# Kernel optimization log

Hardware: AMD Instinct MI355X
Metric: run time of the kernel (lower is better)

The kernel has to match this reference:

```python
import jax, jax.numpy as jnp
import numpy as np

N_NODES = 100000
N_EDGES = 600000
IN_DIM = 128
EDGE_DIM = 32
HIDDEN = 128
NUM_CLASSES = 2


def _glorot(key, shape):
    fan_in, fan_out = shape[0], shape[1]
    lim = float(np.sqrt(6.0 / (fan_in + fan_out)))
    return jax.random.uniform(key, shape, jnp.float32, -lim, lim)


def setup_inputs() -> dict:
    key = jax.random.key(0)
    ks = jax.random.split(key, 16)
    inp = {
        "x": jax.random.normal(ks[0], (N_NODES, IN_DIM), jnp.float32),
        "edge_index": jax.random.randint(ks[1], (2, N_EDGES), 0, N_NODES, jnp.int64),
        "edge_attr": jax.random.normal(ks[2], (N_EDGES, EDGE_DIM), jnp.float32),
        # SAGEConv layer 1 (edge-aware): edge proj, neighbor lin, self lin
        "We1": _glorot(ks[3], (EDGE_DIM, IN_DIM)),
        "be1": jnp.zeros((IN_DIM,), jnp.float32),
        "Wl1": _glorot(ks[4], (IN_DIM, HIDDEN)),
        "bl1": jnp.zeros((HIDDEN,), jnp.float32),
        "Wr1": _glorot(ks[5], (IN_DIM, HIDDEN)),
        "br1": jnp.zeros((HIDDEN,), jnp.float32),
        # SAGEConv layer 2
        "We2": _glorot(ks[6], (EDGE_DIM, HIDDEN)),
        "be2": jnp.zeros((HIDDEN,), jnp.float32),
        "Wl2": _glorot(ks[7], (HIDDEN, HIDDEN)),
        "bl2": jnp.zeros((HIDDEN,), jnp.float32),
        "Wr2": _glorot(ks[8], (HIDDEN, HIDDEN)),
        "br2": jnp.zeros((HIDDEN,), jnp.float32),
        # Edge MLP predictor: Linear(2*hidden, hidden) -> ReLU -> Linear(hidden, num_classes)
        "Wp1": _glorot(ks[9], (2 * HIDDEN, HIDDEN)),
        "bp1": jnp.zeros((HIDDEN,), jnp.float32),
        "Wp2": _glorot(ks[10], (HIDDEN, NUM_CLASSES)),
        "bp2": jnp.zeros((NUM_CLASSES,), jnp.float32),
    }
    return inp


def _sage_conv(x, src, dst, edge_attr, We, be, Wl, bl, Wr, br):
    # Edge-aware message: m_ij = x_j + proj(e_ij); mean-aggregate over dst;
    # out_i = mean_agg @ Wl + x_i @ Wr  (GraphSAGE mean aggregator with edge fusion)
    msg = x[src] + edge_attr @ We + be                       # [E, d]
    agg = jax.ops.segment_sum(msg, dst, num_segments=N_NODES)  # [N, d]
    deg = jax.ops.segment_sum(jnp.ones((msg.shape[0],), msg.dtype), dst, num_segments=N_NODES)
    mean = agg / jnp.maximum(deg, 1.0)[:, None]
    return mean @ Wl + bl + x @ Wr + br


def reference(x, edge_index, edge_attr,
              We1, be1, Wl1, bl1, Wr1, br1,
              We2, be2, Wl2, bl2, Wr2, br2,
              Wp1, bp1, Wp2, bp2):
    src, dst = edge_index[0], edge_index[1]
    h = jax.nn.relu(_sage_conv(x, src, dst, edge_attr, We1, be1, Wl1, bl1, Wr1, br1))
    h = jax.nn.relu(_sage_conv(h, src, dst, edge_attr, We2, be2, Wl2, bl2, Wr2, br2))
    # Edge predictor: gather endpoints, concat, MLP -> logits [E, num_classes]
    he = jnp.concatenate([h[src], h[dst]], axis=-1)
    return jax.nn.relu(he @ Wp1 + bp1) @ Wp2 + bp2
```

## Files before the change

kernel.cpp:

```cpp
#include <hip/hip_runtime.h>

#define N_NODES 100000
#define N_EDGES 600000
#define IN_DIM 128
#define EDGE_DIM 32
#define HIDDEN 128
#define NUM_CLASSES 2
#define NBLK 391

typedef __attribute__((ext_vector_type(4))) float f32x4;
typedef _Float16 f16x2 __attribute__((ext_vector_type(2)));
typedef _Float16 f16x4 __attribute__((ext_vector_type(4)));
typedef _Float16 f16x8 __attribute__((ext_vector_type(8)));

__global__ void hist_kernel(const int* __restrict__ dst, int* __restrict__ cnt) {
    int e = blockIdx.x * blockDim.x + threadIdx.x;
    if (e < N_EDGES) atomicAdd(&cnt[dst[e]], 1);
}

__global__ void scan1_kernel(const int* __restrict__ cnt,
                             int* __restrict__ scanout, int* __restrict__ bsum) {
    __shared__ int s[256];
    int tid = threadIdx.x;
    int i = blockIdx.x * 256 + tid;
    int v = (i < N_NODES) ? cnt[i] : 0;
    s[tid] = v;
    __syncthreads();
#pragma unroll
    for (int off = 1; off < 256; off <<= 1) {
        int t = 0;
        if (tid >= off) t = s[tid - off];
        __syncthreads();
        if (tid >= off) s[tid] += t;
        __syncthreads();
    }
    if (i < N_NODES) scanout[i] = s[tid];
    if (tid == 255) bsum[blockIdx.x] = s[255];
}

__global__ void scan2_kernel(int* __restrict__ bsum) {
    __shared__ int s[512];
    int tid = threadIdx.x;
    int v = (tid < NBLK) ? bsum[tid] : 0;
    s[tid] = v;
    __syncthreads();
#pragma unroll
    for (int off = 1; off < 512; off <<= 1) {
        int t = 0;
        if (tid >= off) t = s[tid - off];
        __syncthreads();
        if (tid >= off) s[tid] += t;
        __syncthreads();
    }
    if (tid < NBLK) bsum[tid] = s[tid] - v;
}

__global__ void scan3_kernel(const int* __restrict__ cnt,
                             const int* __restrict__ scanout,
                             const int* __restrict__ bsum,
                             int* __restrict__ rowptr, int* __restrict__ cur) {
    int i = blockIdx.x * 256 + threadIdx.x;
    if (i < N_NODES) {
        int excl = scanout[i] + bsum[i >> 8] - cnt[i];
        rowptr[i] = excl;
        cur[i] = excl;
    }
    if (i == 0) rowptr[N_NODES] = N_EDGES;
}

__global__ void fill_kernel(const int* __restrict__ src, const int* __restrict__ dst,
                            int* __restrict__ cur, int2* __restrict__ pk,
                            int* __restrict__ pdst) {
    int e = blockIdx.x * blockDim.x + threadIdx.x;
    if (e < N_EDGES) {
        int d = dst[e];
        int pos = atomicAdd(&cur[d], 1);
        int2 v;
        v.x = src[e];
        v.y = e;
        pk[pos] = v;
        pdst[pos] = d;
    }
}

__global__ void xb_kernel(const float* __restrict__ x, _Float16* __restrict__ xb) {
    int i = blockIdx.x * 256 + threadIdx.x;
    if (i < N_NODES * HIDDEN / 2) {
        float2 v = ((const float2*)x)[i];
        f16x2 o;
        o.x = (_Float16)v.x;
        o.y = (_Float16)v.y;
        *(f16x2*)&xb[i * 2] = o;
    }
}

__global__ void wewl_kernel(const float* __restrict__ We, const float* __restrict__ be,
                            const float* __restrict__ Wl,
                            float* __restrict__ WeWl, float* __restrict__ beWl) {
    int idx = blockIdx.x * 256 + threadIdx.x;
    if (idx >= 33 * 128) return;
    int r = idx >> 7;
    int n = idx & 127;
    float s = 0.f;
    if (r < 32) {
        for (int j = 0; j < 128; ++j) s += We[r * 128 + j] * Wl[j * 128 + n];
        WeWl[r * 128 + n] = s;
    } else {
        for (int j = 0; j < 128; ++j) s += be[j] * Wl[j * 128 + n];
        beWl[n] = s;
    }
}

__global__ void wbig_swizzle_kernel(const float* __restrict__ Wl,
                                    const float* __restrict__ Wr,
                                    const float* __restrict__ WeWl,
                                    _Float16* __restrict__ Wbs) {
    int idx = blockIdx.x * 256 + threadIdx.x;
    if (idx >= 8 * 9 * 64 * 8) return;
    int j = idx & 7;
    int lane = (idx >> 3) & 63;
    int rem = idx >> 9;
    int ks = rem % 9;
    int nt = rem / 9;
    int k = ks * 32 + ((lane >> 4) & 3) * 8 + j;
    int n = nt * 16 + (lane & 15);
    float v = (k < 128) ? Wl[k * 128 + n]
            : (k < 256) ? Wr[(k - 128) * 128 + n]
                        : WeWl[(k - 256) * 128 + n];
    Wbs[idx] = (_Float16)v;
}

template <bool EA>
__global__ __launch_bounds__(256) void agg_kernel_t(const _Float16* __restrict__ xin,
                                                    const int* __restrict__ rowptr,
                                                    const int2* __restrict__ pk,
                                                    const float* __restrict__ ea,
                                                    _Float16* __restrict__ meanb,
                                                    _Float16* __restrict__ eamb) {
    int wid = blockIdx.x * 4 + (threadIdx.x >> 6);
    int lane = threadIdx.x & 63;
    int node = lane >> 3;
    int slot = lane & 7;
    int half = lane >> 5;
    int k = lane & 31;
    int n0 = wid * 8;

    int rp = rowptr[n0 + (lane < 9 ? lane : 8)];
    int s_n = __shfl(rp, node);
    int e_n = __shfl(rp, node + 1);
    int c_n = e_n - s_n; c_n = c_n > 8 ? 8 : c_n;
    int pos = s_n + (slot < c_n ? slot : 0);
    pos = pos < N_EDGES ? pos : N_EDGES - 1;
    int2 pv = pk[pos];

    float accx[8], accy[8], eacc[8];
#pragma unroll
    for (int i = 0; i < 8; ++i) {
        accx[i] = 0.f; accy[i] = 0.f;
        if (EA) eacc[i] = 0.f;
    }

#pragma unroll
    for (int i = 0; i < 8; ++i) {
        int di = __shfl(rp, i + 1) - __shfl(rp, i);
        int ci = di > 8 ? 8 : di;
        f16x2 r[8];
#pragma unroll
        for (int u = 0; u < 8; ++u) {
            int s = __shfl(pv.x, i * 8 + u);
            r[u] = *(const f16x2*)&xin[s * HIDDEN + lane * 2];
        }
        float g[4];
        if (EA) {
#pragma unroll
            for (int up = 0; up < 4; ++up) {
                int eid = __shfl(pv.y, i * 8 + 2 * up + half);
                g[up] = ea[eid * EDGE_DIM + k];
            }
        }
#pragma unroll
        for (int u = 0; u < 8; ++u)
            if (u < ci) { accx[i] += (float)r[u].x; accy[i] += (float)r[u].y; }
        if (EA) {
#pragma unroll
            for (int up = 0; up < 4; ++up)
                if (2 * up + half < ci) eacc[i] += g[up];
        }
    }

#pragma unroll
    for (int i = 0; i < 8; ++i) {
        int si = __shfl(rp, i);
        int ei = __shfl(rp, i + 1);
        int p = si + 8;
        if (p < ei) {
            do {
                int c = ei - p; c = c > 8 ? 8 : c;
                int2 pv2 = pk[p + (slot < c ? slot : 0)];
                f16x2 r[8];
#pragma unroll
                for (int u = 0; u < 8; ++u) {
                    int s = __shfl(pv2.x, u);
                    r[u] = *(const f16x2*)&xin[s * HIDDEN + lane * 2];
                }
                float g[4];
                if (EA) {
#pragma unroll
                    for (int up = 0; up < 4; ++up) {
                        int eid = __shfl(pv2.y, 2 * up + half);
                        g[up] = ea[eid * EDGE_DIM + k];
                    }
                }
#pragma unroll
                for (int u = 0; u < 8; ++u)
                    if (u < c) { accx[i] += (float)r[u].x; accy[i] += (float)r[u].y; }
                if (EA) {
#pragma unroll
                    for (int up = 0; up < 4; ++up)
                        if (2 * up + half < c) eacc[i] += g[up];
                }
                p += c;
            } while (p < ei);
        }
    }

    float dinv[8];
#pragma unroll
    for (int i = 0; i < 8; ++i) {
        int di = __shfl(rp, i + 1) - __shfl(rp, i);
        dinv[i] = 1.f / (float)(di > 1 ? di : 1);
    }
#pragma unroll
    for (int i = 0; i < 8; ++i) {
        f16x2 o;
        o.x = (_Float16)(accx[i] * dinv[i]);
        o.y = (_Float16)(accy[i] * dinv[i]);
        *(f16x2*)&meanb[(n0 + i) * HIDDEN + lane * 2] = o;
    }
    if (EA) {
#pragma unroll
        for (int i = 0; i < 8; ++i) eacc[i] += __shfl_xor(eacc[i], 32);
#pragma unroll
        for (int j = 0; j < 4; ++j) {
            float v  = half ? eacc[4 + j] : eacc[j];
            float dv = half ? dinv[4 + j] : dinv[j];
            int i = half * 4 + j;
            eamb[(n0 + i) * EDGE_DIM + k] = (_Float16)(v * dv);
        }
    }
}

#define APITCH 296
__global__ __launch_bounds__(256) void node_gemm_kernel(
        const _Float16* __restrict__ meanb,
        const _Float16* __restrict__ xb,
        const _Float16* __restrict__ eamb,
        const _Float16* __restrict__ Wbs,
        const int* __restrict__ rowptr,
        const float* __restrict__ bl, const float* __restrict__ br,
        const float* __restrict__ beWl,
        _Float16* __restrict__ outb) {
    __shared__ _Float16 s_a[64 * APITCH];
    __shared__ float s_bias[128];
    __shared__ float s_bw[128];
    __shared__ int s_deg[64];
    int t = threadIdx.x;
    int n0 = blockIdx.x * 64;

    if (t < 128) {
        s_bias[t] = bl[t] + br[t];
        s_bw[t] = beWl[t];
    } else if (t < 192) {
        int m = t - 128;
        int n = n0 + m;
        n = n < N_NODES ? n : N_NODES - 1;
        s_deg[m] = rowptr[n + 1] - rowptr[n];
    }
    for (int i = t; i < 64 * 16; i += 256) {
        int row = i >> 4, seg = i & 15;
        int n = n0 + row;
        n = n < N_NODES ? n : N_NODES - 1;
        *(f16x8*)&s_a[row * APITCH + seg * 8] = *(const f16x8*)&meanb[n * HIDDEN + seg * 8];
        *(f16x8*)&s_a[row * APITCH + 128 + seg * 8] = *(const f16x8*)&xb[n * HIDDEN + seg * 8];
    }
    for (int i = t; i < 64 * 4; i += 256) {
        int row = i >> 2, seg = i & 3;
        int n = n0 + row;
        n = n < N_NODES ? n : N_NODES - 1;
        *(f16x8*)&s_a[row * APITCH + 256 + seg * 8] = *(const f16x8*)&eamb[n * EDGE_DIM + seg * 8];
    }
    __syncthreads();

    int wave = t >> 6;
    int lane = t & 63;
    int col = lane & 15;
    int kgrp = lane >> 4;

    f32x4 acc[8];
#pragma unroll
    for (int nt = 0; nt < 8; ++nt) acc[nt] = (f32x4){0.f, 0.f, 0.f, 0.f};

    const f16x8* __restrict__ Wb = (const f16x8*)Wbs;
#pragma unroll
    for (int ks = 0; ks < 9; ++ks) {
        f16x8 afrag = *(const f16x8*)&s_a[(wave * 16 + col) * APITCH + ks * 32 + kgrp * 8];
#pragma unroll
        for (int nt = 0; nt < 8; ++nt) {
            f16x8 bfrag = Wb[(nt * 9 + ks) * 64 + lane];
            acc[nt] = __builtin_amdgcn_mfma_f32_16x16x32_f16(afrag, bfrag, acc[nt], 0, 0, 0);
        }
    }

#pragma unroll
    for (int nt = 0; nt < 8; ++nt) {
        int feat = nt * 16 + col;
        float b = s_bias[feat];
        float bw = s_bw[feat];
#pragma unroll
        for (int r = 0; r < 4; ++r) {
            int m = wave * 16 + kgrp * 4 + r;
            int n = n0 + m;
            float v = acc[nt][r] + b + (s_deg[m] > 0 ? bw : 0.f);
            v = v > 0.f ? v : 0.f;
            if (n < N_NODES) outb[n * HIDDEN + feat] = (_Float16)v;
        }
    }
}

__global__ void wp1uv_swizzle_kernel(const float* __restrict__ Wp1,
                                     _Float16* __restrict__ Wuv) {
    int idx = blockIdx.x * 256 + threadIdx.x;
    if (idx >= 32768) return;
    int j = idx & 7;
    int lane = (idx >> 3) & 63;
    int ks = (idx >> 9) & 3;
    int nt = (idx >> 11) & 15;
    int k = ks * 32 + ((lane >> 4) & 3) * 8 + j;
    int n = nt * 16 + (lane & 15);
    float v = (n < 128) ? Wp1[k * 128 + n] : Wp1[(128 + k) * 128 + (n - 128)];
    Wuv[idx] = (_Float16)v;
}

#define UPITCH 136
__global__ __launch_bounds__(256) void uv_gemm_kernel(
        const _Float16* __restrict__ h,
        const _Float16* __restrict__ Wuv,
        const float* __restrict__ bp1,
        _Float16* __restrict__ UV) {
    __shared__ _Float16 s_a[64 * UPITCH];
    __shared__ float s_bias[256];
    int t = threadIdx.x;
    int n0 = blockIdx.x * 64;

    s_bias[t] = (t < 128) ? bp1[t] : 0.f;
    for (int i = t; i < 64 * 16; i += 256) {
        int row = i >> 4, seg = i & 15;
        int n = n0 + row;
        n = n < N_NODES ? n : N_NODES - 1;
        *(f16x8*)&s_a[row * UPITCH + seg * 8] = *(const f16x8*)&h[n * HIDDEN + seg * 8];
    }
    __syncthreads();

    int wave = t >> 6;
    int lane = t & 63;
    int col = lane & 15;
    int kgrp = lane >> 4;

    f32x4 acc[16];
#pragma unroll
    for (int nt = 0; nt < 16; ++nt) acc[nt] = (f32x4){0.f, 0.f, 0.f, 0.f};

    const f16x8* __restrict__ Wb = (const f16x8*)Wuv;
#pragma unroll
    for (int ks = 0; ks < 4; ++ks) {
        f16x8 afrag = *(const f16x8*)&s_a[(wave * 16 + col) * UPITCH + ks * 32 + kgrp * 8];
#pragma unroll
        for (int nt = 0; nt < 16; ++nt) {
            f16x8 bfrag = Wb[(nt * 4 + ks) * 64 + lane];
            acc[nt] = __builtin_amdgcn_mfma_f32_16x16x32_f16(afrag, bfrag, acc[nt], 0, 0, 0);
        }
    }

#pragma unroll
    for (int nt = 0; nt < 16; ++nt) {
        int feat = nt * 16 + col;
        float b = s_bias[feat];
#pragma unroll
        for (int r = 0; r < 4; ++r) {
            int m = wave * 16 + kgrp * 4 + r;
            int n = n0 + m;
            if (n < N_NODES) UV[n * 256 + feat] = (_Float16)(acc[nt][r] + b);
        }
    }
}

__global__ __launch_bounds__(256) void edge_pred_kernel(
        const _Float16* __restrict__ UV,
        const int2* __restrict__ pk,
        const int* __restrict__ pdst,
        const float* __restrict__ Wp2,
        const float* __restrict__ bp2,
        float* __restrict__ out) {
    int t = threadIdx.x;
    int wave = t >> 6;
    int lane = t & 63;
    int slot = lane >> 5;
    int k4 = (lane & 31) * 4;

    float4 wa = *(const float4*)&Wp2[k4 * 2];
    float4 wb = *(const float4*)&Wp2[k4 * 2 + 4];
    float b0 = bp2[0], b1 = bp2[1];

    int e0 = blockIdx.x * 32 + wave * 8;

    int2 pv[4];
    int dn[4];
#pragma unroll
    for (int u = 0; u < 4; ++u) {
        int pos = e0 + 2 * u + slot;
        pv[u] = pk[pos];
        dn[u] = pdst[pos];
    }
    f16x4 uu[4], vv[4];
#pragma unroll
    for (int u = 0; u < 4; ++u) {
        uu[u] = *(const f16x4*)&UV[pv[u].x * 256 + k4];
        vv[u] = *(const f16x4*)&UV[dn[u] * 256 + 128 + k4];
    }

    float p0[4], p1[4];
#pragma unroll
    for (int u = 0; u < 4; ++u) {
        float z0 = (float)uu[u].x + (float)vv[u].x; z0 = z0 > 0.f ? z0 : 0.f;
        float z1 = (float)uu[u].y + (float)vv[u].y; z1 = z1 > 0.f ? z1 : 0.f;
        float z2 = (float)uu[u].z + (float)vv[u].z; z2 = z2 > 0.f ? z2 : 0.f;
        float z3 = (float)uu[u].w + (float)vv[u].w; z3 = z3 > 0.f ? z3 : 0.f;
        p0[u] = z0 * wa.x + z1 * wa.z + z2 * wb.x + z3 * wb.z;
        p1[u] = z0 * wa.y + z1 * wa.w + z2 * wb.y + z3 * wb.w;
    }
#pragma unroll
    for (int m = 1; m < 32; m <<= 1) {
#pragma unroll
        for (int u = 0; u < 4; ++u) {
            p0[u] += __shfl_xor(p0[u], m);
            p1[u] += __shfl_xor(p1[u], m);
        }
    }
    if ((lane & 31) == 0) {
#pragma unroll
        for (int u = 0; u < 4; ++u) {
            float2 o;
            o.x = p0[u] + b0;
            o.y = p1[u] + b1;
            *(float2*)&out[pv[u].y * 2] = o;
        }
    }
}

extern "C" void kernel_launch(void* const* d_in, const int* in_sizes, int n_in,
                              void* d_out, int out_size, void* d_ws, size_t ws_size,
                              hipStream_t stream) {
    const float* x   = (const float*)d_in[0];
    const int*   ei  = (const int*)d_in[1];
    const float* ea  = (const float*)d_in[2];
    const float* We1 = (const float*)d_in[3];
    const float* be1 = (const float*)d_in[4];
    const float* Wl1 = (const float*)d_in[5];
    const float* bl1 = (const float*)d_in[6];
    const float* Wr1 = (const float*)d_in[7];
    const float* br1 = (const float*)d_in[8];
    const float* We2 = (const float*)d_in[9];
    const float* be2 = (const float*)d_in[10];
    const float* Wl2 = (const float*)d_in[11];
    const float* bl2 = (const float*)d_in[12];
    const float* Wr2 = (const float*)d_in[13];
    const float* br2 = (const float*)d_in[14];
    const float* Wp1 = (const float*)d_in[15];
    const float* bp1 = (const float*)d_in[16];
    const float* Wp2 = (const float*)d_in[17];
    const float* bp2 = (const float*)d_in[18];
    float* out = (float*)d_out;

    const int* src = ei;
    const int* dst = ei + N_EDGES;

    char* ws = (char*)d_ws;
    int*   cnt     = (int*)(ws + 0);
    int*   scanout = (int*)(ws + 409600);
    int*   bsum    = (int*)(ws + 819200);
    int*   rowptr  = (int*)(ws + 827392);
    int*   cur     = (int*)(ws + 1236992);
    int2*  pk      = (int2*)(ws + 1646592);
    float* WeWl1   = (float*)(ws + 6447104);
    float* beWl1   = (float*)(ws + 6463488);
    float* WeWl2   = (float*)(ws + 6464000);
    float* beWl2   = (float*)(ws + 6480384);
    _Float16* eamb = (_Float16*)(ws + 6480896);
    _Float16* xb   = (_Float16*)(ws + 12880896);
    _Float16* meanb= (_Float16*)(ws + 38480896);
    _Float16* UV   = (_Float16*)(ws + 12880896);
    _Float16* h1b  = (_Float16*)(ws + 64080896);
    _Float16* h2b  = (_Float16*)(ws + 89680896);
    _Float16* Wbs1 = (_Float16*)(ws + 115280896);
    _Float16* Wbs2 = (_Float16*)(ws + 115354624);
    _Float16* Wuv  = (_Float16*)(ws + 115428352);
    int*   pdst    = (int*)(ws + 115493888);

    const int EB = (N_EDGES + 255) / 256;

    hipMemsetAsync(cnt, 0, N_NODES * sizeof(int), stream);
    hist_kernel<<<EB, 256, 0, stream>>>(dst, cnt);
    scan1_kernel<<<NBLK, 256, 0, stream>>>(cnt, scanout, bsum);
    scan2_kernel<<<1, 512, 0, stream>>>(bsum);
    scan3_kernel<<<NBLK, 256, 0, stream>>>(cnt, scanout, bsum, rowptr, cur);
    fill_kernel<<<EB, 256, 0, stream>>>(src, dst, cur, pk, pdst);

    wewl_kernel<<<17, 256, 0, stream>>>(We1, be1, Wl1, WeWl1, beWl1);
    wewl_kernel<<<17, 256, 0, stream>>>(We2, be2, Wl2, WeWl2, beWl2);
    xb_kernel<<<(N_NODES * HIDDEN / 2 + 255) / 256, 256, 0, stream>>>(x, xb);
    wbig_swizzle_kernel<<<144, 256, 0, stream>>>(Wl1, Wr1, WeWl1, Wbs1);
    wbig_swizzle_kernel<<<144, 256, 0, stream>>>(Wl2, Wr2, WeWl2, Wbs2);
    wp1uv_swizzle_kernel<<<128, 256, 0, stream>>>(Wp1, Wuv);

    agg_kernel_t<true><<<N_NODES / 32, 256, 0, stream>>>(xb, rowptr, pk, ea, meanb, eamb);
    node_gemm_kernel<<<(N_NODES + 63) / 64, 256, 0, stream>>>(
        meanb, xb, eamb, Wbs1, rowptr, bl1, br1, beWl1, h1b);

    agg_kernel_t<false><<<N_NODES / 32, 256, 0, stream>>>(h1b, rowptr, pk, nullptr, meanb, nullptr);
    node_gemm_kernel<<<(N_NODES + 63) / 64, 256, 0, stream>>>(
        meanb, h1b, eamb, Wbs2, rowptr, bl2, br2, beWl2, h2b);

    uv_gemm_kernel<<<(N_NODES + 63) / 64, 256, 0, stream>>>(h2b, Wuv, bp1, UV);
    edge_pred_kernel<<<N_EDGES / 32, 256, 0, stream>>>(UV, pk, pdst, Wp2, bp2, out);
}
```

Measured before the change: 495.7 us.

## Fuse neighbor aggregation into node GEMM and use MFMA for edge predictor

Merges the separate mean-aggregation and node GEMM kernels into one per-layer kernel that writes the aggregated means straight into shared memory. This removes the meanb global round trip and two launches. The edge predictor's second linear layer is now a padded 16x16x32 MFMA over a pre-swizzled fp16 Wp2 instead of per-lane dot products with shuffle reductions. The trade-offs are fewer waves doing the gather per node-GEMM block, which lowers parallelism in the latency-bound gather, and extra fp16 rounding of the ReLU activations in the predictor.

```diff
diff --git a/kernel.cpp b/kernel.cpp
--- a/kernel.cpp
+++ b/kernel.cpp
@@ -130,133 +130,15 @@
     Wbs[idx] = (_Float16)v;
 }
 
+#define APITCH 296
 template <bool EA>
-__global__ __launch_bounds__(256) void agg_kernel_t(const _Float16* __restrict__ xin,
-                                                    const int* __restrict__ rowptr,
-                                                    const int2* __restrict__ pk,
-                                                    const float* __restrict__ ea,
-                                                    _Float16* __restrict__ meanb,
-                                                    _Float16* __restrict__ eamb) {
-    int wid = blockIdx.x * 4 + (threadIdx.x >> 6);
-    int lane = threadIdx.x & 63;
-    int node = lane >> 3;
-    int slot = lane & 7;
-    int half = lane >> 5;
-    int k = lane & 31;
-    int n0 = wid * 8;
-
-    int rp = rowptr[n0 + (lane < 9 ? lane : 8)];
-    int s_n = __shfl(rp, node);
-    int e_n = __shfl(rp, node + 1);
-    int c_n = e_n - s_n; c_n = c_n > 8 ? 8 : c_n;
-    int pos = s_n + (slot < c_n ? slot : 0);
-    pos = pos < N_EDGES ? pos : N_EDGES - 1;
-    int2 pv = pk[pos];
-
-    float accx[8], accy[8], eacc[8];
-#pragma unroll
-    for (int i = 0; i < 8; ++i) {
-        accx[i] = 0.f; accy[i] = 0.f;
-        if (EA) eacc[i] = 0.f;
-    }
-
-#pragma unroll
-    for (int i = 0; i < 8; ++i) {
-        int di = __shfl(rp, i + 1) - __shfl(rp, i);
-        int ci = di > 8 ? 8 : di;
-        f16x2 r[8];
-#pragma unroll
-        for (int u = 0; u < 8; ++u) {
-            int s = __shfl(pv.x, i * 8 + u);
-            r[u] = *(const f16x2*)&xin[s * HIDDEN + lane * 2];
-        }
-        float g[4];
-        if (EA) {
-#pragma unroll
-            for (int up = 0; up < 4; ++up) {
-                int eid = __shfl(pv.y, i * 8 + 2 * up + half);
-                g[up] = ea[eid * EDGE_DIM + k];
-            }
-        }
-#pragma unroll
-        for (int u = 0; u < 8; ++u)
-            if (u < ci) { accx[i] += (float)r[u].x; accy[i] += (float)r[u].y; }
-        if (EA) {
-#pragma unroll
-            for (int up = 0; up < 4; ++up)
-                if (2 * up + half < ci) eacc[i] += g[up];
-        }
-    }
-
-#pragma unroll
-    for (int i = 0; i < 8; ++i) {
-        int si = __shfl(rp, i);
-        int ei = __shfl(rp, i + 1);
-        int p = si + 8;
-        if (p < ei) {
-            do {
-                int c = ei - p; c = c > 8 ? 8 : c;
-                int2 pv2 = pk[p + (slot < c ? slot : 0)];
-                f16x2 r[8];
-#pragma unroll
-                for (int u = 0; u < 8; ++u) {
-                    int s = __shfl(pv2.x, u);
-                    r[u] = *(const f16x2*)&xin[s * HIDDEN + lane * 2];
-                }
-                float g[4];
-                if (EA) {
-#pragma unroll
-                    for (int up = 0; up < 4; ++up) {
-                        int eid = __shfl(pv2.y, 2 * up + half);
-                        g[up] = ea[eid * EDGE_DIM + k];
-                    }
-                }
-#pragma unroll
-                for (int u = 0; u < 8; ++u)
-                    if (u < c) { accx[i] += (float)r[u].x; accy[i] += (float)r[u].y; }
-                if (EA) {
-#pragma unroll
-                    for (int up = 0; up < 4; ++up)
-                        if (2 * up + half < c) eacc[i] += g[up];
-                }
-                p += c;
-            } while (p < ei);
-        }
-    }
-
-    float dinv[8];
-#pragma unroll
-    for (int i = 0; i < 8; ++i) {
-        int di = __shfl(rp, i + 1) - __shfl(rp, i);
-        dinv[i] = 1.f / (float)(di > 1 ? di : 1);
-    }
-#pragma unroll
-    for (int i = 0; i < 8; ++i) {
-        f16x2 o;
-        o.x = (_Float16)(accx[i] * dinv[i]);
-        o.y = (_Float16)(accy[i] * dinv[i]);
-        *(f16x2*)&meanb[(n0 + i) * HIDDEN + lane * 2] = o;
-    }
-    if (EA) {
-#pragma unroll
-        for (int i = 0; i < 8; ++i) eacc[i] += __shfl_xor(eacc[i], 32);
-#pragma unroll
-        for (int j = 0; j < 4; ++j) {
-            float v  = half ? eacc[4 + j] : eacc[j];
-            float dv = half ? dinv[4 + j] : dinv[j];
-            int i = half * 4 + j;
-            eamb[(n0 + i) * EDGE_DIM + k] = (_Float16)(v * dv);
-        }
-    }
-}
-
-#define APITCH 296
-__global__ __launch_bounds__(256) void node_gemm_kernel(
-        const _Float16* __restrict__ meanb,
-        const _Float16* __restrict__ xb,
-        const _Float16* __restrict__ eamb,
+__global__ __launch_bounds__(256) void fused_layer_kernel(
+        const _Float16* __restrict__ xin,
+        const int* __restrict__ rowptr,
+        const int2* __restrict__ pk,
+        const float* __restrict__ ea,
+        _Float16* __restrict__ eamb,
         const _Float16* __restrict__ Wbs,
-        const int* __restrict__ rowptr,
         const float* __restrict__ bl, const float* __restrict__ br,
         const float* __restrict__ beWl,
         _Float16* __restrict__ outb) {
@@ -266,33 +148,150 @@
     __shared__ int s_deg[64];
     int t = threadIdx.x;
     int n0 = blockIdx.x * 64;
-
-    if (t < 128) {
-        s_bias[t] = bl[t] + br[t];
-        s_bw[t] = beWl[t];
-    } else if (t < 192) {
-        int m = t - 128;
-        int n = n0 + m;
-        n = n < N_NODES ? n : N_NODES - 1;
-        s_deg[m] = rowptr[n + 1] - rowptr[n];
-    }
+    int wave = t >> 6;
+    int lane = t & 63;
+
+    if (t < 128) { s_bias[t] = bl[t] + br[t]; s_bw[t] = beWl[t]; }
+
     for (int i = t; i < 64 * 16; i += 256) {
         int row = i >> 4, seg = i & 15;
-        int n = n0 + row;
-        n = n < N_NODES ? n : N_NODES - 1;
-        *(f16x8*)&s_a[row * APITCH + seg * 8] = *(const f16x8*)&meanb[n * HIDDEN + seg * 8];
-        *(f16x8*)&s_a[row * APITCH + 128 + seg * 8] = *(const f16x8*)&xb[n * HIDDEN + seg * 8];
-    }
-    for (int i = t; i < 64 * 4; i += 256) {
-        int row = i >> 2, seg = i & 3;
-        int n = n0 + row;
-        n = n < N_NODES ? n : N_NODES - 1;
-        *(f16x8*)&s_a[row * APITCH + 256 + seg * 8] = *(const f16x8*)&eamb[n * EDGE_DIM + seg * 8];
+        int n = n0 + row; n = n < N_NODES ? n : N_NODES - 1;
+        *(f16x8*)&s_a[row * APITCH + 128 + seg * 8] = *(const f16x8*)&xin[n * HIDDEN + seg * 8];
+    }
+    if (!EA) {
+        for (int i = t; i < 64 * 4; i += 256) {
+            int row = i >> 2, seg = i & 3;
+            int n = n0 + row; n = n < N_NODES ? n : N_NODES - 1;
+            *(f16x8*)&s_a[row * APITCH + 256 + seg * 8] = *(const f16x8*)&eamb[n * EDGE_DIM + seg * 8];
+        }
+    }
+
+    int node = lane >> 3;
+    int slot = lane & 7;
+    int half = lane >> 5;
+    int kk = lane & 31;
+
+#pragma unroll 1
+    for (int g = 0; g < 2; ++g) {
+        int ng = n0 + wave * 16 + g * 8;
+        int rpi = ng + (lane < 9 ? lane : 8);
+        rpi = rpi < N_NODES ? rpi : N_NODES;
+        int rp = rowptr[rpi];
+        int s_n = __shfl(rp, node);
+        int e_n = __shfl(rp, node + 1);
+        int c_n = e_n - s_n; c_n = c_n > 8 ? 8 : c_n;
+        int pos = s_n + (slot < c_n ? slot : 0);
+        pos = pos < N_EDGES ? pos : N_EDGES - 1;
+        int2 pv = pk[pos];
+
+        float accx[8], accy[8], eacc[8];
+#pragma unroll
+        for (int i = 0; i < 8; ++i) {
+            accx[i] = 0.f; accy[i] = 0.f;
+            if (EA) eacc[i] = 0.f;
+        }
+
+#pragma unroll
+        for (int i = 0; i < 8; ++i) {
+            int di = __shfl(rp, i + 1) - __shfl(rp, i);
+            int ci = di > 8 ? 8 : di;
+            f16x2 r[8];
+#pragma unroll
+            for (int u = 0; u < 8; ++u) {
+                int s = __shfl(pv.x, i * 8 + u);
+                r[u] = *(const f16x2*)&xin[s * HIDDEN + lane * 2];
+            }
+            float gg[4];
+            if (EA) {
+#pragma unroll
+                for (int up = 0; up < 4; ++up) {
+                    int eid = __shfl(pv.y, i * 8 + 2 * up + half);
+                    gg[up] = ea[eid * EDGE_DIM + kk];
+                }
+            }
+#pragma unroll
+            for (int u = 0; u < 8; ++u)
+                if (u < ci) { accx[i] += (float)r[u].x; accy[i] += (float)r[u].y; }
+            if (EA) {
+#pragma unroll
+                for (int up = 0; up < 4; ++up)
+                    if (2 * up + half < ci) eacc[i] += gg[up];
+            }
+        }
+
+#pragma unroll
+        for (int i = 0; i < 8; ++i) {
+            int si = __shfl(rp, i);
+            int ei2 = __shfl(rp, i + 1);
+            int p = si + 8;
+            if (p < ei2) {
+                do {
+                    int c = ei2 - p; c = c > 8 ? 8 : c;
+                    int2 pv2 = pk[p + (slot < c ? slot : 0)];
+                    f16x2 r[8];
+#pragma unroll
+                    for (int u = 0; u < 8; ++u) {
+                        int s = __shfl(pv2.x, u);
+                        r[u] = *(const f16x2*)&xin[s * HIDDEN + lane * 2];
+                    }
+                    float gg[4];
+                    if (EA) {
+#pragma unroll
+                        for (int up = 0; up < 4; ++up) {
+                            int eid = __shfl(pv2.y, 2 * up + half);
+                            gg[up] = ea[eid * EDGE_DIM + kk];
+                        }
+                    }
+#pragma unroll
+                    for (int u = 0; u < 8; ++u)
+                        if (u < c) { accx[i] += (float)r[u].x; accy[i] += (float)r[u].y; }
+                    if (EA) {
+#pragma unroll
+                        for (int up = 0; up < 4; ++up)
+                            if (2 * up + half < c) eacc[i] += gg[up];
+                    }
+                    p += c;
+                } while (p < ei2);
+            }
+        }
+
+        float dinv[8];
+#pragma unroll
+        for (int i = 0; i < 8; ++i) {
+            int di = __shfl(rp, i + 1) - __shfl(rp, i);
+            dinv[i] = 1.f / (float)(di > 1 ? di : 1);
+        }
+#pragma unroll
+        for (int i = 0; i < 8; ++i) {
+            int row = wave * 16 + g * 8 + i;
+            f16x2 o;
+            o.x = (_Float16)(accx[i] * dinv[i]);
+            o.y = (_Float16)(accy[i] * dinv[i]);
+            *(f16x2*)&s_a[row * APITCH + lane * 2] = o;
+        }
+        {
+            int li = lane < 8 ? lane : 0;
+            int dd = __shfl(rp, li + 1) - __shfl(rp, li);
+            if (lane < 8) s_deg[wave * 16 + g * 8 + lane] = dd;
+        }
+        if (EA) {
+#pragma unroll
+            for (int i = 0; i < 8; ++i) eacc[i] += __shfl_xor(eacc[i], 32);
+#pragma unroll
+            for (int j = 0; j < 4; ++j) {
+                float v  = half ? eacc[4 + j] : eacc[j];
+                float dv = half ? dinv[4 + j] : dinv[j];
+                int i = half * 4 + j;
+                int row = wave * 16 + g * 8 + i;
+                _Float16 hv = (_Float16)(v * dv);
+                s_a[row * APITCH + 256 + kk] = hv;
+                int nn = ng + i;
+                if (nn < N_NODES) eamb[nn * EDGE_DIM + kk] = hv;
+            }
+        }
     }
     __syncthreads();
 
-    int wave = t >> 6;
-    int lane = t & 63;
     int col = lane & 15;
     int kgrp = lane >> 4;
 
@@ -328,17 +327,28 @@
 }
 
 __global__ void wp1uv_swizzle_kernel(const float* __restrict__ Wp1,
-                                     _Float16* __restrict__ Wuv) {
+                                     const float* __restrict__ Wp2,
+                                     _Float16* __restrict__ Wuv,
+                                     _Float16* __restrict__ Wp2b) {
     int idx = blockIdx.x * 256 + threadIdx.x;
-    if (idx >= 32768) return;
-    int j = idx & 7;
-    int lane = (idx >> 3) & 63;
-    int ks = (idx >> 9) & 3;
-    int nt = (idx >> 11) & 15;
-    int k = ks * 32 + ((lane >> 4) & 3) * 8 + j;
-    int n = nt * 16 + (lane & 15);
-    float v = (n < 128) ? Wp1[k * 128 + n] : Wp1[(128 + k) * 128 + (n - 128)];
-    Wuv[idx] = (_Float16)v;
+    if (idx < 32768) {
+        int j = idx & 7;
+        int lane = (idx >> 3) & 63;
+        int ks = (idx >> 9) & 3;
+        int nt = (idx >> 11) & 15;
+        int k = ks * 32 + ((lane >> 4) & 3) * 8 + j;
+        int n = nt * 16 + (lane & 15);
+        float v = (n < 128) ? Wp1[k * 128 + n] : Wp1[(128 + k) * 128 + (n - 128)];
+        Wuv[idx] = (_Float16)v;
+    } else if (idx < 32768 + 2048) {
+        int r = idx - 32768;
+        int j = r & 7;
+        int lane = (r >> 3) & 63;
+        int ks = r >> 9;
+        int k = ks * 32 + ((lane >> 4) & 3) * 8 + j;
+        int col = lane & 15;
+        Wp2b[r] = (col < 2) ? (_Float16)Wp2[k * 2 + col] : (_Float16)0;
+    }
 }
 
 #define UPITCH 136
@@ -398,62 +408,47 @@
         const _Float16* __restrict__ UV,
         const int2* __restrict__ pk,
         const int* __restrict__ pdst,
-        const float* __restrict__ Wp2,
+        const _Float16* __restrict__ Wp2b,
         const float* __restrict__ bp2,
         float* __restrict__ out) {
     int t = threadIdx.x;
     int wave = t >> 6;
     int lane = t & 63;
-    int slot = lane >> 5;
-    int k4 = (lane & 31) * 4;
-
-    float4 wa = *(const float4*)&Wp2[k4 * 2];
-    float4 wb = *(const float4*)&Wp2[k4 * 2 + 4];
-    float b0 = bp2[0], b1 = bp2[1];
-
-    int e0 = blockIdx.x * 32 + wave * 8;
-
-    int2 pv[4];
-    int dn[4];
-#pragma unroll
-    for (int u = 0; u < 4; ++u) {
-        int pos = e0 + 2 * u + slot;
-        pv[u] = pk[pos];
-        dn[u] = pdst[pos];
-    }
-    f16x4 uu[4], vv[4];
-#pragma unroll
-    for (int u = 0; u < 4; ++u) {
-        uu[u] = *(const f16x4*)&UV[pv[u].x * 256 + k4];
-        vv[u] = *(const f16x4*)&UV[dn[u] * 256 + 128 + k4];
-    }
-
-    float p0[4], p1[4];
-#pragma unroll
-    for (int u = 0; u < 4; ++u) {
-        float z0 = (float)uu[u].x + (float)vv[u].x; z0 = z0 > 0.f ? z0 : 0.f;
-        float z1 = (float)uu[u].y + (float)vv[u].y; z1 = z1 > 0.f ? z1 : 0.f;
-        float z2 = (float)uu[u].z + (float)vv[u].z; z2 = z2 > 0.f ? z2 : 0.f;
-        float z3 = (float)uu[u].w + (float)vv[u].w; z3 = z3 > 0.f ? z3 : 0.f;
-        p0[u] = z0 * wa.x + z1 * wa.z + z2 * wb.x + z3 * wb.z;
-        p1[u] = z0 * wa.y + z1 * wa.w + z2 * wb.y + z3 * wb.w;
-    }
-#pragma unroll
-    for (int m = 1; m < 32; m <<= 1) {
-#pragma unroll
-        for (int u = 0; u < 4; ++u) {
-            p0[u] += __shfl_xor(p0[u], m);
-            p1[u] += __shfl_xor(p1[u], m);
-        }
-    }
-    if ((lane & 31) == 0) {
-#pragma unroll
-        for (int u = 0; u < 4; ++u) {
-            float2 o;
-            o.x = p0[u] + b0;
-            o.y = p1[u] + b1;
-            *(float2*)&out[pv[u].y * 2] = o;
-        }
+    int row = lane & 15;
+    int kgrp = lane >> 4;
+    int e0 = blockIdx.x * 64 + wave * 16;
+
+    int2 pv = pk[e0 + row];
+    int dn = pdst[e0 + row];
+    const _Float16* ubase = &UV[pv.x * 256 + kgrp * 8];
+    const _Float16* vbase = &UV[dn * 256 + 128 + kgrp * 8];
+
+    f16x8 au[4], av[4], bf[4];
+#pragma unroll
+    for (int ks = 0; ks < 4; ++ks) {
+        au[ks] = *(const f16x8*)&ubase[ks * 32];
+        av[ks] = *(const f16x8*)&vbase[ks * 32];
+        bf[ks] = *(const f16x8*)&Wp2b[(ks * 64 + lane) * 8];
+    }
+
+    f32x4 acc = (f32x4){0.f, 0.f, 0.f, 0.f};
+#pragma unroll
+    for (int ks = 0; ks < 4; ++ks) {
+        f16x8 z = au[ks] + av[ks];
+#pragma unroll
+        for (int j = 0; j < 8; ++j) z[j] = z[j] > (_Float16)0 ? z[j] : (_Float16)0;
+        acc = __builtin_amdgcn_mfma_f32_16x16x32_f16(z, bf[ks], acc, 0, 0, 0);
+    }
+
+    int eids[4];
+#pragma unroll
+    for (int r = 0; r < 4; ++r) eids[r] = __shfl(pv.y, kgrp * 4 + r);
+
+    int col = lane & 15;
+    if (col < 2) {
+        float bb = bp2[col];
+#pragma unroll
+        for (int r = 0; r < 4; ++r) out[eids[r] * 2 + col] = acc[r] + bb;
     }
 }
 
@@ -497,7 +492,6 @@
     float* beWl2   = (float*)(ws + 6480384);
     _Float16* eamb = (_Float16*)(ws + 6480896);
     _Float16* xb   = (_Float16*)(ws + 12880896);
-    _Float16* meanb= (_Float16*)(ws + 38480896);
     _Float16* UV   = (_Float16*)(ws + 12880896);
     _Float16* h1b  = (_Float16*)(ws + 64080896);
     _Float16* h2b  = (_Float16*)(ws + 89680896);
@@ -505,6 +499,7 @@
     _Float16* Wbs2 = (_Float16*)(ws + 115354624);
     _Float16* Wuv  = (_Float16*)(ws + 115428352);
     int*   pdst    = (int*)(ws + 115493888);
+    _Float16* Wp2b = (_Float16*)(ws + 409600);
 
     const int EB = (N_EDGES + 255) / 256;
 
@@ -520,16 +515,14 @@
     xb_kernel<<<(N_NODES * HIDDEN / 2 + 255) / 256, 256, 0, stream>>>(x, xb);
     wbig_swizzle_kernel<<<144, 256, 0, stream>>>(Wl1, Wr1, WeWl1, Wbs1);
     wbig_swizzle_kernel<<<144, 256, 0, stream>>>(Wl2, Wr2, WeWl2, Wbs2);
-    wp1uv_swizzle_kernel<<<128, 256, 0, stream>>>(Wp1, Wuv);
-
-    agg_kernel_t<true><<<N_NODES / 32, 256, 0, stream>>>(xb, rowptr, pk, ea, meanb, eamb);
-    node_gemm_kernel<<<(N_NODES + 63) / 64, 256, 0, stream>>>(
-        meanb, xb, eamb, Wbs1, rowptr, bl1, br1, beWl1, h1b);
-
-    agg_kernel_t<false><<<N_NODES / 32, 256, 0, stream>>>(h1b, rowptr, pk, nullptr, meanb, nullptr);
-    node_gemm_kernel<<<(N_NODES + 63) / 64, 256, 0, stream>>>(
-        meanb, h1b, eamb, Wbs2, rowptr, bl2, br2, beWl2, h2b);
+    wp1uv_swizzle_kernel<<<136, 256, 0, stream>>>(Wp1, Wp2, Wuv, Wp2b);
+
+    fused_layer_kernel<true><<<(N_NODES + 63) / 64, 256, 0, stream>>>(
+        xb, rowptr, pk, ea, eamb, Wbs1, bl1, br1, beWl1, h1b);
+
+    fused_layer_kernel<false><<<(N_NODES + 63) / 64, 256, 0, stream>>>(
+        h1b, rowptr, pk, nullptr, eamb, Wbs2, bl2, br2, beWl2, h2b);
 
     uv_gemm_kernel<<<(N_NODES + 63) / 64, 256, 0, stream>>>(h2b, Wuv, bp1, UV);
-    edge_pred_kernel<<<N_EDGES / 32, 256, 0, stream>>>(UV, pk, pdst, Wp2, bp2, out);
-}
+    edge_pred_kernel<<<N_EDGES / 64, 256, 0, stream>>>(UV, pk, pdst, Wp2b, bp2, out);
+}
```

New measurement: 549.9 us. +10.9%, slower.

## Fuse layer-2 node GEMM with UV projection and split U/V buffers

Applied to the files above, without the earlier changes.

Fuses the second SAGE node GEMM with the edge-predictor UV projection so h2 stays in shared memory instead of being written and re-read from global memory. U and V are written to separate contiguous 128-wide arrays, so each edge gather reads from a denser buffer. The per-layer weight preprocessing kernels are also merged into single launches covering both layers. The fused kernel holds both accumulator sets, which raises register pressure and may lower occupancy.

```diff
diff --git a/kernel.cpp b/kernel.cpp
--- a/kernel.cpp
+++ b/kernel.cpp
@@ -94,11 +94,21 @@
     }
 }
 
-__global__ void wewl_kernel(const float* __restrict__ We, const float* __restrict__ be,
-                            const float* __restrict__ Wl,
-                            float* __restrict__ WeWl, float* __restrict__ beWl) {
-    int idx = blockIdx.x * 256 + threadIdx.x;
-    if (idx >= 33 * 128) return;
+__global__ void wewl2_kernel(const float* __restrict__ We1, const float* __restrict__ be1,
+                             const float* __restrict__ Wl1,
+                             const float* __restrict__ We2, const float* __restrict__ be2,
+                             const float* __restrict__ Wl2,
+                             float* __restrict__ WeWl1, float* __restrict__ beWl1,
+                             float* __restrict__ WeWl2, float* __restrict__ beWl2) {
+    int idx0 = blockIdx.x * 256 + threadIdx.x;
+    if (idx0 >= 2 * 33 * 128) return;
+    int layer = idx0 >= 33 * 128;
+    int idx = idx0 - layer * 33 * 128;
+    const float* We = layer ? We2 : We1;
+    const float* be = layer ? be2 : be1;
+    const float* Wl = layer ? Wl2 : Wl1;
+    float* WeWl = layer ? WeWl2 : WeWl1;
+    float* beWl = layer ? beWl2 : beWl1;
     int r = idx >> 7;
     int n = idx & 127;
     float s = 0.f;
@@ -111,12 +121,18 @@
     }
 }
 
-__global__ void wbig_swizzle_kernel(const float* __restrict__ Wl,
-                                    const float* __restrict__ Wr,
-                                    const float* __restrict__ WeWl,
-                                    _Float16* __restrict__ Wbs) {
-    int idx = blockIdx.x * 256 + threadIdx.x;
-    if (idx >= 8 * 9 * 64 * 8) return;
+__global__ void wbig2_kernel(const float* __restrict__ Wl1, const float* __restrict__ Wr1,
+                             const float* __restrict__ WeWl1, _Float16* __restrict__ Wbs1,
+                             const float* __restrict__ Wl2, const float* __restrict__ Wr2,
+                             const float* __restrict__ WeWl2, _Float16* __restrict__ Wbs2) {
+    int idx0 = blockIdx.x * 256 + threadIdx.x;
+    if (idx0 >= 2 * 36864) return;
+    int layer = idx0 >= 36864;
+    int idx = idx0 - layer * 36864;
+    const float* Wl = layer ? Wl2 : Wl1;
+    const float* Wr = layer ? Wr2 : Wr1;
+    const float* WeWl = layer ? WeWl2 : WeWl1;
+    _Float16* Wbs = layer ? Wbs2 : Wbs1;
     int j = idx & 7;
     int lane = (idx >> 3) & 63;
     int rem = idx >> 9;
@@ -327,6 +343,131 @@
     }
 }
 
+#define UPITCH 136
+__global__ __launch_bounds__(256) void node_gemm_uv_kernel(
+        const _Float16* __restrict__ meanb,
+        const _Float16* __restrict__ h1,
+        const _Float16* __restrict__ eamb,
+        const _Float16* __restrict__ Wbs,
+        const int* __restrict__ rowptr,
+        const float* __restrict__ bl, const float* __restrict__ br,
+        const float* __restrict__ beWl,
+        const _Float16* __restrict__ Wuv,
+        const float* __restrict__ bp1,
+        _Float16* __restrict__ U,
+        _Float16* __restrict__ V) {
+    __shared__ _Float16 s_a[64 * APITCH];
+    __shared__ float s_bias[128];
+    __shared__ float s_bw[128];
+    __shared__ int s_deg[64];
+    int t = threadIdx.x;
+    int n0 = blockIdx.x * 64;
+
+    if (t < 128) {
+        s_bias[t] = bl[t] + br[t];
+        s_bw[t] = beWl[t];
+    } else if (t < 192) {
+        int m = t - 128;
+        int n = n0 + m;
+        n = n < N_NODES ? n : N_NODES - 1;
+        s_deg[m] = rowptr[n + 1] - rowptr[n];
+    }
+    for (int i = t; i < 64 * 16; i += 256) {
+        int row = i >> 4, seg = i & 15;
+        int n = n0 + row;
+        n = n < N_NODES ? n : N_NODES - 1;
+        *(f16x8*)&s_a[row * APITCH + seg * 8] = *(const f16x8*)&meanb[n * HIDDEN + seg * 8];
+        *(f16x8*)&s_a[row * APITCH + 128 + seg * 8] = *(const f16x8*)&h1[n * HIDDEN + seg * 8];
+    }
+    for (int i = t; i < 64 * 4; i += 256) {
+        int row = i >> 2, seg = i & 3;
+        int n = n0 + row;
+        n = n < N_NODES ? n : N_NODES - 1;
+        *(f16x8*)&s_a[row * APITCH + 256 + seg * 8] = *(const f16x8*)&eamb[n * EDGE_DIM + seg * 8];
+    }
+    __syncthreads();
+
+    int wave = t >> 6;
+    int lane = t & 63;
+    int col = lane & 15;
+    int kgrp = lane >> 4;
+
+    f32x4 acc[8];
+#pragma unroll
+    for (int nt = 0; nt < 8; ++nt) acc[nt] = (f32x4){0.f, 0.f, 0.f, 0.f};
+
+    const f16x8* __restrict__ Wb = (const f16x8*)Wbs;
+#pragma unroll
+    for (int ks = 0; ks < 9; ++ks) {
+        f16x8 afrag = *(const f16x8*)&s_a[(wave * 16 + col) * APITCH + ks * 32 + kgrp * 8];
+#pragma unroll
+        for (int nt = 0; nt < 8; ++nt) {
+            f16x8 bfrag = Wb[(nt * 9 + ks) * 64 + lane];
+            acc[nt] = __builtin_amdgcn_mfma_f32_16x16x32_f16(afrag, bfrag, acc[nt], 0, 0, 0);
+        }
+    }
+
+    f16x4 h2v[8];
+#pragma unroll
+    for (int nt = 0; nt < 8; ++nt) {
+        int feat = nt * 16 + col;
+        float b = s_bias[feat];
+        float bw = s_bw[feat];
+#pragma unroll
+        for (int r = 0; r < 4; ++r) {
+            int m = wave * 16 + kgrp * 4 + r;
+            float v = acc[nt][r] + b + (s_deg[m] > 0 ? bw : 0.f);
+            v = v > 0.f ? v : 0.f;
+            h2v[nt][r] = (_Float16)v;
+        }
+    }
+
+    __syncthreads();
+    _Float16* s_h = s_a;
+#pragma unroll
+    for (int nt = 0; nt < 8; ++nt) {
+        int feat = nt * 16 + col;
+#pragma unroll
+        for (int r = 0; r < 4; ++r) {
+            int m = wave * 16 + kgrp * 4 + r;
+            s_h[m * UPITCH + feat] = h2v[nt][r];
+        }
+    }
+    if (t < 128) s_bias[t] = bp1[t];
+    __syncthreads();
+
+    f32x4 acc2[16];
+#pragma unroll
+    for (int nt = 0; nt < 16; ++nt) acc2[nt] = (f32x4){0.f, 0.f, 0.f, 0.f};
+
+    const f16x8* __restrict__ Wb2 = (const f16x8*)Wuv;
+#pragma unroll
+    for (int ks = 0; ks < 4; ++ks) {
+        f16x8 afrag = *(const f16x8*)&s_h[(wave * 16 + col) * UPITCH + ks * 32 + kgrp * 8];
+#pragma unroll
+        for (int nt = 0; nt < 16; ++nt) {
+            f16x8 bfrag = Wb2[(nt * 4 + ks) * 64 + lane];
+            acc2[nt] = __builtin_amdgcn_mfma_f32_16x16x32_f16(afrag, bfrag, acc2[nt], 0, 0, 0);
+        }
+    }
+
+#pragma unroll
+    for (int nt = 0; nt < 16; ++nt) {
+        int feat = nt * 16 + col;
+        float b = (nt < 8) ? s_bias[feat] : 0.f;
+#pragma unroll
+        for (int r = 0; r < 4; ++r) {
+            int m = wave * 16 + kgrp * 4 + r;
+            int n = n0 + m;
+            if (n < N_NODES) {
+                _Float16 o = (_Float16)(acc2[nt][r] + b);
+                if (nt < 8) U[n * 128 + feat] = o;
+                else        V[n * 128 + (feat - 128)] = o;
+            }
+        }
+    }
+}
+
 __global__ void wp1uv_swizzle_kernel(const float* __restrict__ Wp1,
                                      _Float16* __restrict__ Wuv) {
     int idx = blockIdx.x * 256 + threadIdx.x;
@@ -341,61 +482,9 @@
     Wuv[idx] = (_Float16)v;
 }
 
-#define UPITCH 136
-__global__ __launch_bounds__(256) void uv_gemm_kernel(
-        const _Float16* __restrict__ h,
-        const _Float16* __restrict__ Wuv,
-        const float* __restrict__ bp1,
-        _Float16* __restrict__ UV) {
-    __shared__ _Float16 s_a[64 * UPITCH];
-    __shared__ float s_bias[256];
-    int t = threadIdx.x;
-    int n0 = blockIdx.x * 64;
-
-    s_bias[t] = (t < 128) ? bp1[t] : 0.f;
-    for (int i = t; i < 64 * 16; i += 256) {
-        int row = i >> 4, seg = i & 15;
-        int n = n0 + row;
-        n = n < N_NODES ? n : N_NODES - 1;
-        *(f16x8*)&s_a[row * UPITCH + seg * 8] = *(const f16x8*)&h[n * HIDDEN + seg * 8];
-    }
-    __syncthreads();
-
-    int wave = t >> 6;
-    int lane = t & 63;
-    int col = lane & 15;
-    int kgrp = lane >> 4;
-
-    f32x4 acc[16];
-#pragma unroll
-    for (int nt = 0; nt < 16; ++nt) acc[nt] = (f32x4){0.f, 0.f, 0.f, 0.f};
-
-    const f16x8* __restrict__ Wb = (const f16x8*)Wuv;
-#pragma unroll
-    for (int ks = 0; ks < 4; ++ks) {
-        f16x8 afrag = *(const f16x8*)&s_a[(wave * 16 + col) * UPITCH + ks * 32 + kgrp * 8];
-#pragma unroll
-        for (int nt = 0; nt < 16; ++nt) {
-            f16x8 bfrag = Wb[(nt * 4 + ks) * 64 + lane];
-            acc[nt] = __builtin_amdgcn_mfma_f32_16x16x32_f16(afrag, bfrag, acc[nt], 0, 0, 0);
-        }
-    }
-
-#pragma unroll
-    for (int nt = 0; nt < 16; ++nt) {
-        int feat = nt * 16 + col;
-        float b = s_bias[feat];
-#pragma unroll
-        for (int r = 0; r < 4; ++r) {
-            int m = wave * 16 + kgrp * 4 + r;
-            int n = n0 + m;
-            if (n < N_NODES) UV[n * 256 + feat] = (_Float16)(acc[nt][r] + b);
-        }
-    }
-}
-
 __global__ __launch_bounds__(256) void edge_pred_kernel(
-        const _Float16* __restrict__ UV,
+        const _Float16* __restrict__ U,
+        const _Float16* __restrict__ V,
         const int2* __restrict__ pk,
         const int* __restrict__ pdst,
         const float* __restrict__ Wp2,
@@ -424,8 +513,8 @@
     f16x4 uu[4], vv[4];
 #pragma unroll
     for (int u = 0; u < 4; ++u) {
-        uu[u] = *(const f16x4*)&UV[pv[u].x * 256 + k4];
-        vv[u] = *(const f16x4*)&UV[dn[u] * 256 + 128 + k4];
+        uu[u] = *(const f16x4*)&U[pv[u].x * 128 + k4];
+        vv[u] = *(const f16x4*)&V[dn[u] * 128 + k4];
     }
 
     float p0[4], p1[4];
@@ -498,9 +587,9 @@
     _Float16* eamb = (_Float16*)(ws + 6480896);
     _Float16* xb   = (_Float16*)(ws + 12880896);
     _Float16* meanb= (_Float16*)(ws + 38480896);
-    _Float16* UV   = (_Float16*)(ws + 12880896);
     _Float16* h1b  = (_Float16*)(ws + 64080896);
-    _Float16* h2b  = (_Float16*)(ws + 89680896);
+    _Float16* U    = (_Float16*)(ws + 12880896);
+    _Float16* V    = (_Float16*)(ws + 89680896);
     _Float16* Wbs1 = (_Float16*)(ws + 115280896);
     _Float16* Wbs2 = (_Float16*)(ws + 115354624);
     _Float16* Wuv  = (_Float16*)(ws + 115428352);
@@ -515,11 +604,11 @@
     scan3_kernel<<<NBLK, 256, 0, stream>>>(cnt, scanout, bsum, rowptr, cur);
     fill_kernel<<<EB, 256, 0, stream>>>(src, dst, cur, pk, pdst);
 
-    wewl_kernel<<<17, 256, 0, stream>>>(We1, be1, Wl1, WeWl1, beWl1);
-    wewl_kernel<<<17, 256, 0, stream>>>(We2, be2, Wl2, WeWl2, beWl2);
+    wewl2_kernel<<<33, 256, 0, stream>>>(We1, be1, Wl1, We2, be2, Wl2,
+                                         WeWl1, beWl1, WeWl2, beWl2);
     xb_kernel<<<(N_NODES * HIDDEN / 2 + 255) / 256, 256, 0, stream>>>(x, xb);
-    wbig_swizzle_kernel<<<144, 256, 0, stream>>>(Wl1, Wr1, WeWl1, Wbs1);
-    wbig_swizzle_kernel<<<144, 256, 0, stream>>>(Wl2, Wr2, WeWl2, Wbs2);
+    wbig2_kernel<<<288, 256, 0, stream>>>(Wl1, Wr1, WeWl1, Wbs1,
+                                          Wl2, Wr2, WeWl2, Wbs2);
     wp1uv_swizzle_kernel<<<128, 256, 0, stream>>>(Wp1, Wuv);
 
     agg_kernel_t<true><<<N_NODES / 32, 256, 0, stream>>>(xb, rowptr, pk, ea, meanb, eamb);
@@ -527,9 +616,8 @@
         meanb, xb, eamb, Wbs1, rowptr, bl1, br1, beWl1, h1b);
 
     agg_kernel_t<false><<<N_NODES / 32, 256, 0, stream>>>(h1b, rowptr, pk, nullptr, meanb, nullptr);
-    node_gemm_kernel<<<(N_NODES + 63) / 64, 256, 0, stream>>>(
-        meanb, h1b, eamb, Wbs2, rowptr, bl2, br2, beWl2, h2b);
-
-    uv_gemm_kernel<<<(N_NODES + 63) / 64, 256, 0, stream>>>(h2b, Wuv, bp1, UV);
-    edge_pred_kernel<<<N_EDGES / 32, 256, 0, stream>>>(UV, pk, pdst, Wp2, bp2, out);
-}
+    node_gemm_uv_kernel<<<(N_NODES + 63) / 64, 256, 0, stream>>>(
+        meanb, h1b, eamb, Wbs2, rowptr, bl2, br2, beWl2, Wuv, bp1, U, V);
+
+    edge_pred_kernel<<<N_EDGES / 32, 256, 0, stream>>>(U, V, pk, pdst, Wp2, bp2, out);
+}
```

After: 516.1 us. 1.04x slower.

## Split node GEMM work by output columns per wave and merge weight-prep launches

Applied to the files above, without the earlier changes.

In the node and UV GEMM kernels, each wave now owns a slice of output columns across all 64 rows instead of 16 rows across all columns. Each B fragment is loaded from global memory once per block rather than by every wave, while A fragments are reread from LDS four times. Separately, the two per-layer weight-precompute kernels and the two weight-swizzle kernels are each merged into one launch to cut launch overhead. Register use for accumulators stays the same, but output stores become less contiguous per wave.

```diff
diff --git a/kernel.cpp b/kernel.cpp
--- a/kernel.cpp
+++ b/kernel.cpp
@@ -94,11 +94,21 @@
     }
 }
 
-__global__ void wewl_kernel(const float* __restrict__ We, const float* __restrict__ be,
-                            const float* __restrict__ Wl,
-                            float* __restrict__ WeWl, float* __restrict__ beWl) {
-    int idx = blockIdx.x * 256 + threadIdx.x;
-    if (idx >= 33 * 128) return;
+__global__ void wewl2_kernel(const float* __restrict__ We1, const float* __restrict__ be1,
+                             const float* __restrict__ Wl1,
+                             const float* __restrict__ We2, const float* __restrict__ be2,
+                             const float* __restrict__ Wl2,
+                             float* __restrict__ WeWl1, float* __restrict__ beWl1,
+                             float* __restrict__ WeWl2, float* __restrict__ beWl2) {
+    int idx0 = blockIdx.x * 256 + threadIdx.x;
+    if (idx0 >= 2 * 33 * 128) return;
+    int layer = idx0 >= 33 * 128;
+    int idx = idx0 - layer * 33 * 128;
+    const float* We = layer ? We2 : We1;
+    const float* be = layer ? be2 : be1;
+    const float* Wl = layer ? Wl2 : Wl1;
+    float* WeWl = layer ? WeWl2 : WeWl1;
+    float* beWl = layer ? beWl2 : beWl1;
     int r = idx >> 7;
     int n = idx & 127;
     float s = 0.f;
@@ -111,12 +121,18 @@
     }
 }
 
-__global__ void wbig_swizzle_kernel(const float* __restrict__ Wl,
-                                    const float* __restrict__ Wr,
-                                    const float* __restrict__ WeWl,
-                                    _Float16* __restrict__ Wbs) {
-    int idx = blockIdx.x * 256 + threadIdx.x;
-    if (idx >= 8 * 9 * 64 * 8) return;
+__global__ void wbig2_kernel(const float* __restrict__ Wl1, const float* __restrict__ Wr1,
+                             const float* __restrict__ WeWl1, _Float16* __restrict__ Wbs1,
+                             const float* __restrict__ Wl2, const float* __restrict__ Wr2,
+                             const float* __restrict__ WeWl2, _Float16* __restrict__ Wbs2) {
+    int idx0 = blockIdx.x * 256 + threadIdx.x;
+    if (idx0 >= 2 * 36864) return;
+    int layer = idx0 >= 36864;
+    int idx = idx0 - layer * 36864;
+    const float* Wl = layer ? Wl2 : Wl1;
+    const float* Wr = layer ? Wr2 : Wr1;
+    const float* WeWl = layer ? WeWl2 : WeWl1;
+    _Float16* Wbs = layer ? Wbs2 : Wbs1;
     int j = idx & 7;
     int lane = (idx >> 3) & 63;
     int rem = idx >> 9;
@@ -296,33 +312,41 @@
     int col = lane & 15;
     int kgrp = lane >> 4;
 
-    f32x4 acc[8];
-#pragma unroll
-    for (int nt = 0; nt < 8; ++nt) acc[nt] = (f32x4){0.f, 0.f, 0.f, 0.f};
+    f32x4 acc[4][2];
+#pragma unroll
+    for (int rt = 0; rt < 4; ++rt) {
+        acc[rt][0] = (f32x4){0.f, 0.f, 0.f, 0.f};
+        acc[rt][1] = (f32x4){0.f, 0.f, 0.f, 0.f};
+    }
 
     const f16x8* __restrict__ Wb = (const f16x8*)Wbs;
 #pragma unroll
     for (int ks = 0; ks < 9; ++ks) {
-        f16x8 afrag = *(const f16x8*)&s_a[(wave * 16 + col) * APITCH + ks * 32 + kgrp * 8];
-#pragma unroll
-        for (int nt = 0; nt < 8; ++nt) {
-            f16x8 bfrag = Wb[(nt * 9 + ks) * 64 + lane];
-            acc[nt] = __builtin_amdgcn_mfma_f32_16x16x32_f16(afrag, bfrag, acc[nt], 0, 0, 0);
-        }
-    }
-
-#pragma unroll
-    for (int nt = 0; nt < 8; ++nt) {
-        int feat = nt * 16 + col;
-        float b = s_bias[feat];
-        float bw = s_bw[feat];
-#pragma unroll
-        for (int r = 0; r < 4; ++r) {
-            int m = wave * 16 + kgrp * 4 + r;
-            int n = n0 + m;
-            float v = acc[nt][r] + b + (s_deg[m] > 0 ? bw : 0.f);
-            v = v > 0.f ? v : 0.f;
-            if (n < N_NODES) outb[n * HIDDEN + feat] = (_Float16)v;
+        f16x8 b0 = Wb[((2 * wave + 0) * 9 + ks) * 64 + lane];
+        f16x8 b1 = Wb[((2 * wave + 1) * 9 + ks) * 64 + lane];
+#pragma unroll
+        for (int rt = 0; rt < 4; ++rt) {
+            f16x8 afrag = *(const f16x8*)&s_a[(rt * 16 + col) * APITCH + ks * 32 + kgrp * 8];
+            acc[rt][0] = __builtin_amdgcn_mfma_f32_16x16x32_f16(afrag, b0, acc[rt][0], 0, 0, 0);
+            acc[rt][1] = __builtin_amdgcn_mfma_f32_16x16x32_f16(afrag, b1, acc[rt][1], 0, 0, 0);
+        }
+    }
+
+#pragma unroll
+    for (int rt = 0; rt < 4; ++rt) {
+#pragma unroll
+        for (int j = 0; j < 2; ++j) {
+            int feat = (2 * wave + j) * 16 + col;
+            float b = s_bias[feat];
+            float bw = s_bw[feat];
+#pragma unroll
+            for (int r = 0; r < 4; ++r) {
+                int m = rt * 16 + kgrp * 4 + r;
+                int n = n0 + m;
+                float v = acc[rt][j][r] + b + (s_deg[m] > 0 ? bw : 0.f);
+                v = v > 0.f ? v : 0.f;
+                if (n < N_NODES) outb[n * HIDDEN + feat] = (_Float16)v;
+            }
         }
     }
 }
@@ -366,30 +390,40 @@
     int col = lane & 15;
     int kgrp = lane >> 4;
 
-    f32x4 acc[16];
-#pragma unroll
-    for (int nt = 0; nt < 16; ++nt) acc[nt] = (f32x4){0.f, 0.f, 0.f, 0.f};
+    f32x4 acc[4][4];
+#pragma unroll
+    for (int rt = 0; rt < 4; ++rt)
+#pragma unroll
+        for (int j = 0; j < 4; ++j) acc[rt][j] = (f32x4){0.f, 0.f, 0.f, 0.f};
 
     const f16x8* __restrict__ Wb = (const f16x8*)Wuv;
 #pragma unroll
     for (int ks = 0; ks < 4; ++ks) {
-        f16x8 afrag = *(const f16x8*)&s_a[(wave * 16 + col) * UPITCH + ks * 32 + kgrp * 8];
-#pragma unroll
-        for (int nt = 0; nt < 16; ++nt) {
-            f16x8 bfrag = Wb[(nt * 4 + ks) * 64 + lane];
-            acc[nt] = __builtin_amdgcn_mfma_f32_16x16x32_f16(afrag, bfrag, acc[nt], 0, 0, 0);
-        }
-    }
-
-#pragma unroll
-    for (int nt = 0; nt < 16; ++nt) {
-        int feat = nt * 16 + col;
-        float b = s_bias[feat];
-#pragma unroll
-        for (int r = 0; r < 4; ++r) {
-            int m = wave * 16 + kgrp * 4 + r;
-            int n = n0 + m;
-            if (n < N_NODES) UV[n * 256 + feat] = (_Float16)(acc[nt][r] + b);
+        f16x8 bf[4];
+#pragma unroll
+        for (int j = 0; j < 4; ++j)
+            bf[j] = Wb[((4 * wave + j) * 4 + ks) * 64 + lane];
+#pragma unroll
+        for (int rt = 0; rt < 4; ++rt) {
+            f16x8 afrag = *(const f16x8*)&s_a[(rt * 16 + col) * UPITCH + ks * 32 + kgrp * 8];
+#pragma unroll
+            for (int j = 0; j < 4; ++j)
+                acc[rt][j] = __builtin_amdgcn_mfma_f32_16x16x32_f16(afrag, bf[j], acc[rt][j], 0, 0, 0);
+        }
+    }
+
+#pragma unroll
+    for (int rt = 0; rt < 4; ++rt) {
+#pragma unroll
+        for (int j = 0; j < 4; ++j) {
+            int feat = (4 * wave + j) * 16 + col;
+            float b = s_bias[feat];
+#pragma unroll
+            for (int r = 0; r < 4; ++r) {
+                int m = rt * 16 + kgrp * 4 + r;
+                int n = n0 + m;
+                if (n < N_NODES) UV[n * 256 + feat] = (_Float16)(acc[rt][j][r] + b);
+            }
         }
     }
 }
@@ -515,11 +549,11 @@
     scan3_kernel<<<NBLK, 256, 0, stream>>>(cnt, scanout, bsum, rowptr, cur);
     fill_kernel<<<EB, 256, 0, stream>>>(src, dst, cur, pk, pdst);
 
-    wewl_kernel<<<17, 256, 0, stream>>>(We1, be1, Wl1, WeWl1, beWl1);
-    wewl_kernel<<<17, 256, 0, stream>>>(We2, be2, Wl2, WeWl2, beWl2);
+    wewl2_kernel<<<33, 256, 0, stream>>>(We1, be1, Wl1, We2, be2, Wl2,
+                                         WeWl1, beWl1, WeWl2, beWl2);
     xb_kernel<<<(N_NODES * HIDDEN / 2 + 255) / 256, 256, 0, stream>>>(x, xb);
-    wbig_swizzle_kernel<<<144, 256, 0, stream>>>(Wl1, Wr1, WeWl1, Wbs1);
-    wbig_swizzle_kernel<<<144, 256, 0, stream>>>(Wl2, Wr2, WeWl2, Wbs2);
+    wbig2_kernel<<<288, 256, 0, stream>>>(Wl1, Wr1, WeWl1, Wbs1,
+                                          Wl2, Wr2, WeWl2, Wbs2);
     wp1uv_swizzle_kernel<<<128, 256, 0, stream>>>(Wp1, Wuv);
 
     agg_kernel_t<true><<<N_NODES / 32, 256, 0, stream>>>(xb, rowptr, pk, ea, meanb, eamb);
```

After: 452.0 us. 1.1x faster.
